# Kernel optimization log

Hardware: AMD Instinct MI355X
Metric: run time of the kernel (lower is better)

## Reference

```python
import jax, jax.numpy as jnp
from jax import lax
import numpy as np

N_ASSETS = 256
BATCH = 512
MAX_WEIGHT = 0.05
N_ITERS = 300       # FISTA iterations (fixed, jit-friendly)
BISECT_ITERS = 60   # bisection iterations for the simplex-box projection
POWER_ITERS = 30    # power iterations for Lipschitz constant


def _project_capped_simplex(v, c):
    """Project rows of v onto {w : sum(w)=1, -c <= w <= c}.

    Finds tau s.t. sum(clip(v - tau, -c, c)) = 1 by bisection (non-diff),
    then recomputes tau exactly from the active-set mask so the projection
    is correctly differentiable (piecewise-linear Jacobian).
    """
    vs = lax.stop_gradient(v)
    lo = jnp.min(vs, axis=-1) - c   # sum = +n*c > 1 here
    hi = jnp.max(vs, axis=-1) + c   # sum = -n*c < 1 here

    def bis(carry, _):
        lo, hi = carry
        mid = 0.5 * (lo + hi)
        s = jnp.sum(jnp.clip(vs - mid[:, None], -c, c), axis=-1)
        lo = jnp.where(s > 1.0, mid, lo)
        hi = jnp.where(s > 1.0, hi, mid)
        return (lo, hi), None

    (lo, hi), _ = lax.scan(bis, (lo, hi), None, length=BISECT_ITERS)
    tau0 = 0.5 * (lo + hi)
    z = vs - tau0[:, None]
    interior = (jnp.abs(z) < c).astype(v.dtype)          # unclipped coords
    k_hi = jnp.sum((z >= c).astype(v.dtype), axis=-1)    # clipped at +c
    k_lo = jnp.sum((z <= -c).astype(v.dtype), axis=-1)   # clipped at -c
    denom = jnp.maximum(jnp.sum(interior, axis=-1), 1.0)
    # exact tau given the (stop-gradient) active set -> correct Jacobian in v
    tau = (jnp.sum(interior * v, axis=-1) + c * (k_hi - k_lo) - 1.0) / denom
    return jnp.clip(v - tau[:, None], -c, c)


def _min_var_weights(covmat_sqrt, c):
    """argmin_w ||A w||^2  s.t. sum(w)=1, -c<=w<=c  (batched FISTA)."""
    B, n, _ = covmat_sqrt.shape
    # Q = A^T A (the objective only depends on A through Q)
    Q = jnp.einsum('bij,bik->bjk', covmat_sqrt, covmat_sqrt)

    # power iteration for lambda_max(Q) -> step size 1/L, L = 2*lambda_max
    u = jnp.ones((B, n), covmat_sqrt.dtype) / jnp.sqrt(jnp.asarray(n, covmat_sqrt.dtype))

    def pit(u, _):
        u = jnp.einsum('bij,bj->bi', Q, u)
        u = u / (jnp.linalg.norm(u, axis=-1, keepdims=True) + 1e-12)
        return u, None

    u, _ = lax.scan(pit, u, None, length=POWER_ITERS)
    lmax = jnp.einsum('bi,bij,bj->b', u, Q, u)
    step = lax.stop_gradient(1.0 / (2.0 * lmax + 1e-12))[:, None]

    w0 = _project_capped_simplex(jnp.full((B, n), 1.0 / n, covmat_sqrt.dtype), c)

    @jax.checkpoint
    def fista(carry, _):
        w, y, t = carry
        g = 2.0 * jnp.einsum('bij,bj->bi', Q, y)
        w_new = _project_capped_simplex(y - step * g, c)
        t_new = 0.5 * (1.0 + jnp.sqrt(1.0 + 4.0 * t * t))
        y_new = w_new + ((t - 1.0) / t_new) * (w_new - w)
        return (w_new, y_new, t_new), None

    t0 = jnp.asarray(1.0, covmat_sqrt.dtype)
    (w, _, _), _ = lax.scan(fista, (w0, w0, t0), None, length=N_ITERS)
    return w


def setup_inputs() -> dict:
    key = jax.random.key(0)
    covmat_sqrt = jax.random.normal(
        key, (BATCH, N_ASSETS, N_ASSETS), dtype=jnp.float32
    ) / np.sqrt(N_ASSETS).astype(np.float32)
    return {"covmat_sqrt": covmat_sqrt}


def reference(covmat_sqrt):
    return _min_var_weights(covmat_sqrt, MAX_WEIGHT)
```

## Files before the change

### kernel.cpp

```cpp
#include <hip/hip_runtime.h>
#include <math.h>


#define NA    256
#define CAPW  0.05f

typedef float v2f __attribute__((ext_vector_type(2)));

template<int CTRL, int RM>
__device__ __forceinline__ float dpp0(float x) {
    return __int_as_float(__builtin_amdgcn_update_dpp(
        0, __float_as_int(x), CTRL, RM, 0xf, true));
}
template<int CTRL, int RM>
__device__ __forceinline__ float dppI(float x, float ident) {
    return __int_as_float(__builtin_amdgcn_update_dpp(
        __float_as_int(ident), __float_as_int(x), CTRL, RM, 0xf, false));
}
__device__ __forceinline__ float bcast63(float x) {
    return __int_as_float(__builtin_amdgcn_readlane(__float_as_int(x), 63));
}
__device__ __forceinline__ float wsum(float x) {
    x += dpp0<0x111, 0xf>(x);
    x += dpp0<0x112, 0xf>(x);
    x += dpp0<0x114, 0xf>(x);
    x += dpp0<0x118, 0xf>(x);
    x += dpp0<0x142, 0xa>(x);
    x += dpp0<0x143, 0xc>(x);
    return bcast63(x);
}
__device__ __forceinline__ float wmin(float x) {
    const float I = 1e30f;
    x = fminf(x, dppI<0x111, 0xf>(x, I));
    x = fminf(x, dppI<0x112, 0xf>(x, I));
    x = fminf(x, dppI<0x114, 0xf>(x, I));
    x = fminf(x, dppI<0x118, 0xf>(x, I));
    x = fminf(x, dppI<0x142, 0xa>(x, I));
    x = fminf(x, dppI<0x143, 0xc>(x, I));
    return bcast63(x);
}
__device__ __forceinline__ float wmax(float x) {
    const float I = -1e30f;
    x = fmaxf(x, dppI<0x111, 0xf>(x, I));
    x = fmaxf(x, dppI<0x112, 0xf>(x, I));
    x = fmaxf(x, dppI<0x114, 0xf>(x, I));
    x = fmaxf(x, dppI<0x118, 0xf>(x, I));
    x = fmaxf(x, dppI<0x142, 0xa>(x, I));
    x = fmaxf(x, dppI<0x143, 0xc>(x, I));
    return bcast63(x);
}

__global__ void __launch_bounds__(512, 2)
markowitz_fista(const float* __restrict__ A, float* __restrict__ out)
{
    __shared__ float A_lds[32 * 256];
    __shared__ float y_lds[256];
    __shared__ float p_lds[8 * 256];
    __shared__ int   done_flag;

    const int tid = threadIdx.x;
    const int b   = blockIdx.x;
    const int r4  = tid & 63;
    const int e   = tid >> 6;
    const int R0  = r4 * 4;
    const int C0  = e * 32;

    const float* __restrict__ Ab = A + (size_t)b * NA * NA;

    v2f q2[4][16];
    #pragma unroll
    for (int a = 0; a < 4; ++a)
        #pragma unroll
        for (int k = 0; k < 16; ++k) q2[a][k] = (v2f){0.0f, 0.0f};

    for (int it = 0; it < 8; ++it) {
        __syncthreads();
        const float4* src = (const float4*)(Ab + it * 32 * 256);
        float4* dst = (float4*)A_lds;
        #pragma unroll
        for (int qd = 0; qd < 4; ++qd) dst[qd * 512 + tid] = src[qd * 512 + tid];
        __syncthreads();
        for (int ii = 0; ii < 32; ++ii) {
            const float* row = A_lds + ii * 256;
            float4 rv = *(const float4*)(row + R0);
            v2f r0 = {rv.x, rv.x}, r1 = {rv.y, rv.y}, r2 = {rv.z, rv.z}, r3 = {rv.w, rv.w};
            #pragma unroll
            for (int cc = 0; cc < 8; ++cc) {
                float4 cv = *(const float4*)(row + C0 + 4 * cc);
                v2f clo = {cv.x, cv.y}, chi = {cv.z, cv.w};
                q2[0][2*cc  ] = __builtin_elementwise_fma(r0, clo, q2[0][2*cc  ]);
                q2[0][2*cc+1] = __builtin_elementwise_fma(r0, chi, q2[0][2*cc+1]);
                q2[1][2*cc  ] = __builtin_elementwise_fma(r1, clo, q2[1][2*cc  ]);
                q2[1][2*cc+1] = __builtin_elementwise_fma(r1, chi, q2[1][2*cc+1]);
                q2[2][2*cc  ] = __builtin_elementwise_fma(r2, clo, q2[2][2*cc  ]);
                q2[2][2*cc+1] = __builtin_elementwise_fma(r2, chi, q2[2][2*cc+1]);
                q2[3][2*cc  ] = __builtin_elementwise_fma(r3, clo, q2[3][2*cc  ]);
                q2[3][2*cc+1] = __builtin_elementwise_fma(r3, chi, q2[3][2*cc+1]);
            }
        }
    }

    auto partials = [&](bool chk) -> bool {
        __syncthreads();
        int fl = chk ? done_flag : 0;
        v2f aL0 = {0,0}, aL1 = {0,0}, aL2 = {0,0}, aL3 = {0,0};
        v2f aH0 = {0,0}, aH1 = {0,0}, aH2 = {0,0}, aH3 = {0,0};
        const float* yv = y_lds + C0;
        #pragma unroll
        for (int cc = 0; cc < 8; ++cc) {
            float4 y4 = *(const float4*)(yv + 4 * cc);
            v2f ylo = {y4.x, y4.y}, yhi = {y4.z, y4.w};
            aL0 = __builtin_elementwise_fma(q2[0][2*cc  ], ylo, aL0);
            aH0 = __builtin_elementwise_fma(q2[0][2*cc+1], yhi, aH0);
            aL1 = __builtin_elementwise_fma(q2[1][2*cc  ], ylo, aL1);
            aH1 = __builtin_elementwise_fma(q2[1][2*cc+1], yhi, aH1);
            aL2 = __builtin_elementwise_fma(q2[2][2*cc  ], ylo, aL2);
            aH2 = __builtin_elementwise_fma(q2[2][2*cc+1], yhi, aH2);
            aL3 = __builtin_elementwise_fma(q2[3][2*cc  ], ylo, aL3);
            aH3 = __builtin_elementwise_fma(q2[3][2*cc+1], yhi, aH3);
        }
        if (fl) return true;
        v2f s0 = aL0 + aH0, s1 = aL1 + aH1, s2 = aL2 + aH2, s3 = aL3 + aH3;
        *(float4*)(p_lds + e * 256 + R0) =
            make_float4(s0.x + s0.y, s1.x + s1.y, s2.x + s2.y, s3.x + s3.y);
        __syncthreads();
        return false;
    };
    auto reduceg = [&]() -> float4 {
        float4 r = *(const float4*)(p_lds + 4 * tid);
        #pragma unroll
        for (int ee = 1; ee < 8; ++ee) {
            float4 pv = *(const float4*)(p_lds + ee * 256 + 4 * tid);
            r.x += pv.x; r.y += pv.y; r.z += pv.z; r.w += pv.w;
        }
        return r;
    };

    if (tid < 64) {
        *(float4*)(y_lds + 4 * tid) = make_float4(0.0625f, 0.0625f, 0.0625f, 0.0625f);
    }
    float u0 = 0.f, u1 = 0.f, u2 = 0.f, u3 = 0.f;
    for (int p = 0; p < 30; ++p) {
        partials(false);
        if (tid < 64) {
            float4 g4 = reduceg();
            float ss = wsum(g4.x*g4.x + g4.y*g4.y + g4.z*g4.z + g4.w*g4.w);
            float inv = 1.0f / (sqrtf(ss) + 1e-12f);
            u0 = g4.x * inv; u1 = g4.y * inv; u2 = g4.z * inv; u3 = g4.w * inv;
            *(float4*)(y_lds + 4 * tid) = make_float4(u0, u1, u2, u3);
        }
    }
    partials(false);

    float step2 = 0.f, t = 1.0f, tau_ws = 0.0f, rm = 0.0f;
    float wa = 0.f, wb = 0.f, wc = 0.f, wd = 0.f;
    float ya = 0.f, yb = 0.f, yc = 0.f, yd = 0.f;
    if (tid < 64) {
        float4 g4 = reduceg();
        float lm = wsum(u0*g4.x + u1*g4.y + u2*g4.z + u3*g4.w);
        float step = 1.0f / (2.0f * lm + 1e-12f);
        step2 = 2.0f * step;
        wa = wb = wc = wd = 1.0f / 256.0f;
        ya = yb = yc = yd = 1.0f / 256.0f;
        *(float4*)(y_lds + 4 * tid) = make_float4(ya, yb, yc, yd);
    }
    if (tid == 0) done_flag = 0;

    for (int itn = 0; itn < 300; ++itn) {
        if (partials(true)) break;
        if (tid < 64) {
            float4 g4 = reduceg();
            float v0 = ya - step2 * g4.x;
            float v1 = yb - step2 * g4.y;
            float v2 = yc - step2 * g4.z;
            float v3 = yd - step2 * g4.w;

            float lo = wmin(fminf(fminf(v0, v1), fminf(v2, v3))) - CAPW;
            float hi = wmax(fmaxf(fmaxf(v0, v1), fmaxf(v2, v3))) + CAPW;
            float tau = fminf(fmaxf(tau_ws, lo), hi);

            float s = 0.f, cnt = 1.f, sm1 = 0.f;
            bool have = false;
            for (int ni = 0; ni < 10; ++ni) {
                float z0 = v0 - tau, z1 = v1 - tau, z2 = v2 - tau, z3 = v3 - tau;
                float c0 = fminf(fmaxf(z0, -CAPW), CAPW);
                float c1 = fminf(fmaxf(z1, -CAPW), CAPW);
                float c2 = fminf(fmaxf(z2, -CAPW), CAPW);
                float c3 = fminf(fmaxf(z3, -CAPW), CAPW);
                s   = wsum(c0 + c1 + c2 + c3);
                cnt = wsum((fabsf(z0) < CAPW ? 1.f : 0.f) +
                           (fabsf(z1) < CAPW ? 1.f : 0.f) +
                           (fabsf(z2) < CAPW ? 1.f : 0.f) +
                           (fabsf(z3) < CAPW ? 1.f : 0.f));
                sm1 = s - 1.0f;
                if (fabsf(sm1) <= 1e-5f) { have = true; break; }
                if (sm1 > 0.0f) lo = tau; else hi = tau;
                float tn2 = tau + sm1 / fmaxf(cnt, 1.0f);
                if (!(tn2 > lo && tn2 < hi)) tn2 = 0.5f * (lo + hi);
                tau = tn2;
            }
            if (!have) {
                float z0 = v0 - tau, z1 = v1 - tau, z2 = v2 - tau, z3 = v3 - tau;
                float c0 = fminf(fmaxf(z0, -CAPW), CAPW);
                float c1 = fminf(fmaxf(z1, -CAPW), CAPW);
                float c2 = fminf(fmaxf(z2, -CAPW), CAPW);
                float c3 = fminf(fmaxf(z3, -CAPW), CAPW);
                s   = wsum(c0 + c1 + c2 + c3);
                cnt = wsum((fabsf(z0) < CAPW ? 1.f : 0.f) +
                           (fabsf(z1) < CAPW ? 1.f : 0.f) +
                           (fabsf(z2) < CAPW ? 1.f : 0.f) +
                           (fabsf(z3) < CAPW ? 1.f : 0.f));
                sm1 = s - 1.0f;
            }
            float tauf = tau + sm1 / fmaxf(cnt, 1.0f);
            tau_ws = tauf;
            float w0n = fminf(fmaxf(v0 - tauf, -CAPW), CAPW);
            float w1n = fminf(fmaxf(v1 - tauf, -CAPW), CAPW);
            float w2n = fminf(fmaxf(v2 - tauf, -CAPW), CAPW);
            float w3n = fminf(fmaxf(v3 - tauf, -CAPW), CAPW);

            float tn = 0.5f * (1.0f + sqrtf(1.0f + 4.0f * t * t));
            float beta = (t - 1.0f) / tn;
            float y0n = w0n + beta * (w0n - wa);
            float y1n = w1n + beta * (w1n - wb);
            float y2n = w2n + beta * (w2n - wc);
            float y3n = w3n + beta * (w3n - wd);

            float dm = fmaxf(fmaxf(fabsf(w0n - wa), fabsf(w1n - wb)),
                             fmaxf(fabsf(w2n - wc), fabsf(w3n - wd)));
            rm = fmaxf(rm, dm);
            if ((itn & 7) == 7) {
                float rmax = wmax(rm);
                if (rmax < 1e-10f && tid == 0) done_flag = 1;
                rm = 0.0f;
            }

            wa = w0n; wb = w1n; wc = w2n; wd = w3n;
            ya = y0n; yb = y1n; yc = y2n; yd = y3n;
            t = tn;
            *(float4*)(y_lds + 4 * tid) = make_float4(ya, yb, yc, yd);
        }
    }

    if (tid < 64) {
        *(float4*)(out + b * 256 + 4 * tid) = make_float4(wa, wb, wc, wd);
    }
}

extern "C" void kernel_launch(void* const* d_in, const int* in_sizes, int n_in,
                              void* d_out, int out_size, void* d_ws, size_t ws_size,
                              hipStream_t stream) {
    (void)in_sizes; (void)n_in; (void)d_ws; (void)ws_size; (void)out_size;
    const float* A = (const float*)d_in[0];
    float* out = (float*)d_out;
    hipLaunchKernelGGL(markowitz_fista, dim3(512), dim3(512), 0, stream, A, out);
}
```

Baseline: 1.056 ms.

## Replicate projection in every wave and double-buffer partials to halve barriers

Every one of the 8 waves now runs the redundant projection and FISTA update itself, so each wave holds the full y vector in registers. The matvec reads y through readlane instead of from LDS. The partial-sum buffer is double-buffered, so each iteration needs one __syncthreads instead of two, and the done-flag broadcast through shared memory is gone. The cost is that all waves execute the serial bisection/Newton projection and the extra readlane instructions, rather than only wave 0 doing it while the others wait.

```diff
diff --git a/kernel.cpp b/kernel.cpp
--- a/kernel.cpp
+++ b/kernel.cpp
@@ -19,6 +19,9 @@
 }
 __device__ __forceinline__ float bcast63(float x) {
     return __int_as_float(__builtin_amdgcn_readlane(__float_as_int(x), 63));
+}
+__device__ __forceinline__ float rlane(float x, int lane) {
+    return __int_as_float(__builtin_amdgcn_readlane(__float_as_int(x), lane));
 }
 __device__ __forceinline__ float wsum(float x) {
     x += dpp0<0x111, 0xf>(x);
@@ -54,9 +57,7 @@
 markowitz_fista(const float* __restrict__ A, float* __restrict__ out)
 {
     __shared__ float A_lds[32 * 256];
-    __shared__ float y_lds[256];
-    __shared__ float p_lds[8 * 256];
-    __shared__ int   done_flag;
+    __shared__ float p_lds[2][8 * 256];
 
     const int tid = threadIdx.x;
     const int b   = blockIdx.x;
@@ -64,6 +65,7 @@
     const int e   = tid >> 6;
     const int R0  = r4 * 4;
     const int C0  = e * 32;
+    const int lb  = __builtin_amdgcn_readfirstlane(e) * 8;
 
     const float* __restrict__ Ab = A + (size_t)b * NA * NA;
 
@@ -100,16 +102,14 @@
         }
     }
 
-    auto partials = [&](bool chk) -> bool {
-        __syncthreads();
-        int fl = chk ? done_flag : 0;
+    auto matvec = [&](float y0, float y1, float y2, float y3, float* buf) {
         v2f aL0 = {0,0}, aL1 = {0,0}, aL2 = {0,0}, aL3 = {0,0};
         v2f aH0 = {0,0}, aH1 = {0,0}, aH2 = {0,0}, aH3 = {0,0};
-        const float* yv = y_lds + C0;
         #pragma unroll
         for (int cc = 0; cc < 8; ++cc) {
-            float4 y4 = *(const float4*)(yv + 4 * cc);
-            v2f ylo = {y4.x, y4.y}, yhi = {y4.z, y4.w};
+            const int L = lb + cc;
+            v2f ylo = { rlane(y0, L), rlane(y1, L) };
+            v2f yhi = { rlane(y2, L), rlane(y3, L) };
             aL0 = __builtin_elementwise_fma(q2[0][2*cc  ], ylo, aL0);
             aH0 = __builtin_elementwise_fma(q2[0][2*cc+1], yhi, aH0);
             aL1 = __builtin_elementwise_fma(q2[1][2*cc  ], ylo, aL1);
@@ -119,131 +119,127 @@
             aL3 = __builtin_elementwise_fma(q2[3][2*cc  ], ylo, aL3);
             aH3 = __builtin_elementwise_fma(q2[3][2*cc+1], yhi, aH3);
         }
-        if (fl) return true;
         v2f s0 = aL0 + aH0, s1 = aL1 + aH1, s2 = aL2 + aH2, s3 = aL3 + aH3;
-        *(float4*)(p_lds + e * 256 + R0) =
+        *(float4*)(buf + e * 256 + R0) =
             make_float4(s0.x + s0.y, s1.x + s1.y, s2.x + s2.y, s3.x + s3.y);
-        __syncthreads();
-        return false;
     };
-    auto reduceg = [&]() -> float4 {
-        float4 r = *(const float4*)(p_lds + 4 * tid);
+    auto reduceg = [&](const float* buf) -> float4 {
+        float4 r = *(const float4*)(buf + R0);
         #pragma unroll
         for (int ee = 1; ee < 8; ++ee) {
-            float4 pv = *(const float4*)(p_lds + ee * 256 + 4 * tid);
+            float4 pv = *(const float4*)(buf + ee * 256 + R0);
             r.x += pv.x; r.y += pv.y; r.z += pv.z; r.w += pv.w;
         }
         return r;
     };
 
+    float u0 = 0.0625f, u1 = 0.0625f, u2 = 0.0625f, u3 = 0.0625f;
+    matvec(u0, u1, u2, u3, p_lds[0]);
+    __syncthreads();
+    int pb = 0;
+    for (int p = 0; p < 30; ++p) {
+        float4 g4 = reduceg(p_lds[pb]);
+        float ss = wsum(g4.x*g4.x + g4.y*g4.y + g4.z*g4.z + g4.w*g4.w);
+        float inv = 1.0f / (sqrtf(ss) + 1e-12f);
+        u0 = g4.x * inv; u1 = g4.y * inv; u2 = g4.z * inv; u3 = g4.w * inv;
+        pb ^= 1;
+        matvec(u0, u1, u2, u3, p_lds[pb]);
+        __syncthreads();
+    }
+    float4 gq = reduceg(p_lds[pb]);
+    float lm = wsum(u0*gq.x + u1*gq.y + u2*gq.z + u3*gq.w);
+    float step  = 1.0f / (2.0f * lm + 1e-12f);
+    float step2 = 2.0f * step;
+
+    float t = 1.0f, tau_ws = 0.0f, rm = 0.0f;
+    float wa = 1.0f/256.0f, wb = 1.0f/256.0f, wc = 1.0f/256.0f, wd = 1.0f/256.0f;
+    float ya = wa, yb = wb, yc = wc, yd = wd;
+
+    pb ^= 1;
+    matvec(ya, yb, yc, yd, p_lds[pb]);
+    __syncthreads();
+
+    for (int itn = 0; itn < 300; ++itn) {
+        float4 g4 = reduceg(p_lds[pb]);
+        float v0 = ya - step2 * g4.x;
+        float v1 = yb - step2 * g4.y;
+        float v2 = yc - step2 * g4.z;
+        float v3 = yd - step2 * g4.w;
+
+        float lo = wmin(fminf(fminf(v0, v1), fminf(v2, v3))) - CAPW;
+        float hi = wmax(fmaxf(fmaxf(v0, v1), fmaxf(v2, v3))) + CAPW;
+        float tau = fminf(fmaxf(tau_ws, lo), hi);
+
+        float s = 0.f, cnt = 1.f, sm1 = 0.f;
+        bool have = false;
+        for (int ni = 0; ni < 10; ++ni) {
+            float z0 = v0 - tau, z1 = v1 - tau, z2 = v2 - tau, z3 = v3 - tau;
+            float c0 = fminf(fmaxf(z0, -CAPW), CAPW);
+            float c1 = fminf(fmaxf(z1, -CAPW), CAPW);
+            float c2 = fminf(fmaxf(z2, -CAPW), CAPW);
+            float c3 = fminf(fmaxf(z3, -CAPW), CAPW);
+            s   = wsum(c0 + c1 + c2 + c3);
+            cnt = wsum((fabsf(z0) < CAPW ? 1.f : 0.f) +
+                       (fabsf(z1) < CAPW ? 1.f : 0.f) +
+                       (fabsf(z2) < CAPW ? 1.f : 0.f) +
+                       (fabsf(z3) < CAPW ? 1.f : 0.f));
+            sm1 = s - 1.0f;
+            if (fabsf(sm1) <= 1e-5f) { have = true; break; }
+            if (sm1 > 0.0f) lo = tau; else hi = tau;
+            float tn2 = tau + sm1 / fmaxf(cnt, 1.0f);
+            if (!(tn2 > lo && tn2 < hi)) tn2 = 0.5f * (lo + hi);
+            tau = tn2;
+        }
+        if (!have) {
+            float z0 = v0 - tau, z1 = v1 - tau, z2 = v2 - tau, z3 = v3 - tau;
+            float c0 = fminf(fmaxf(z0, -CAPW), CAPW);
+            float c1 = fminf(fmaxf(z1, -CAPW), CAPW);
+            float c2 = fminf(fmaxf(z2, -CAPW), CAPW);
+            float c3 = fminf(fmaxf(z3, -CAPW), CAPW);
+            s   = wsum(c0 + c1 + c2 + c3);
+            cnt = wsum((fabsf(z0) < CAPW ? 1.f : 0.f) +
+                       (fabsf(z1) < CAPW ? 1.f : 0.f) +
+                       (fabsf(z2) < CAPW ? 1.f : 0.f) +
+                       (fabsf(z3) < CAPW ? 1.f : 0.f));
+            sm1 = s - 1.0f;
+        }
+        float tauf = tau + sm1 / fmaxf(cnt, 1.0f);
+        tau_ws = tauf;
+        float w0n = fminf(fmaxf(v0 - tauf, -CAPW), CAPW);
+        float w1n = fminf(fmaxf(v1 - tauf, -CAPW), CAPW);
+        float w2n = fminf(fmaxf(v2 - tauf, -CAPW), CAPW);
+        float w3n = fminf(fmaxf(v3 - tauf, -CAPW), CAPW);
+
+        float tn = 0.5f * (1.0f + sqrtf(1.0f + 4.0f * t * t));
+        float beta = (t - 1.0f) / tn;
+        float y0n = w0n + beta * (w0n - wa);
+        float y1n = w1n + beta * (w1n - wb);
+        float y2n = w2n + beta * (w2n - wc);
+        float y3n = w3n + beta * (w3n - wd);
+
+        float dm = fmaxf(fmaxf(fabsf(w0n - wa), fabsf(w1n - wb)),
+                         fmaxf(fabsf(w2n - wc), fabsf(w3n - wd)));
+        rm = fmaxf(rm, dm);
+        bool stop = false;
+        if ((itn & 7) == 7) {
+            float rmax = wmax(rm);
+            stop = (rmax < 1e-10f);
+            rm = 0.0f;
+        }
+
+        wa = w0n; wb = w1n; wc = w2n; wd = w3n;
+        ya = y0n; yb = y1n; yc = y2n; yd = y3n;
+        t = tn;
+
+        if (stop || itn == 299) break;
+
+        pb ^= 1;
+        matvec(ya, yb, yc, yd, p_lds[pb]);
+        __syncthreads();
+    }
+
     if (tid < 64) {
-        *(float4*)(y_lds + 4 * tid) = make_float4(0.0625f, 0.0625f, 0.0625f, 0.0625f);
-    }
-    float u0 = 0.f, u1 = 0.f, u2 = 0.f, u3 = 0.f;
-    for (int p = 0; p < 30; ++p) {
-        partials(false);
-        if (tid < 64) {
-            float4 g4 = reduceg();
-            float ss = wsum(g4.x*g4.x + g4.y*g4.y + g4.z*g4.z + g4.w*g4.w);
-            float inv = 1.0f / (sqrtf(ss) + 1e-12f);
-            u0 = g4.x * inv; u1 = g4.y * inv; u2 = g4.z * inv; u3 = g4.w * inv;
-            *(float4*)(y_lds + 4 * tid) = make_float4(u0, u1, u2, u3);
-        }
-    }
-    partials(false);
-
-    float step2 = 0.f, t = 1.0f, tau_ws = 0.0f, rm = 0.0f;
-    float wa = 0.f, wb = 0.f, wc = 0.f, wd = 0.f;
-    float ya = 0.f, yb = 0.f, yc = 0.f, yd = 0.f;
-    if (tid < 64) {
-        float4 g4 = reduceg();
-        float lm = wsum(u0*g4.x + u1*g4.y + u2*g4.z + u3*g4.w);
-        float step = 1.0f / (2.0f * lm + 1e-12f);
-        step2 = 2.0f * step;
-        wa = wb = wc = wd = 1.0f / 256.0f;
-        ya = yb = yc = yd = 1.0f / 256.0f;
-        *(float4*)(y_lds + 4 * tid) = make_float4(ya, yb, yc, yd);
-    }
-    if (tid == 0) done_flag = 0;
-
-    for (int itn = 0; itn < 300; ++itn) {
-        if (partials(true)) break;
-        if (tid < 64) {
-            float4 g4 = reduceg();
-            float v0 = ya - step2 * g4.x;
-            float v1 = yb - step2 * g4.y;
-            float v2 = yc - step2 * g4.z;
-            float v3 = yd - step2 * g4.w;
-
-            float lo = wmin(fminf(fminf(v0, v1), fminf(v2, v3))) - CAPW;
-            float hi = wmax(fmaxf(fmaxf(v0, v1), fmaxf(v2, v3))) + CAPW;
-            float tau = fminf(fmaxf(tau_ws, lo), hi);
-
-            float s = 0.f, cnt = 1.f, sm1 = 0.f;
-            bool have = false;
-            for (int ni = 0; ni < 10; ++ni) {
-                float z0 = v0 - tau, z1 = v1 - tau, z2 = v2 - tau, z3 = v3 - tau;
-                float c0 = fminf(fmaxf(z0, -CAPW), CAPW);
-                float c1 = fminf(fmaxf(z1, -CAPW), CAPW);
-                float c2 = fminf(fmaxf(z2, -CAPW), CAPW);
-                float c3 = fminf(fmaxf(z3, -CAPW), CAPW);
-                s   = wsum(c0 + c1 + c2 + c3);
-                cnt = wsum((fabsf(z0) < CAPW ? 1.f : 0.f) +
-                           (fabsf(z1) < CAPW ? 1.f : 0.f) +
-                           (fabsf(z2) < CAPW ? 1.f : 0.f) +
-                           (fabsf(z3) < CAPW ? 1.f : 0.f));
-                sm1 = s - 1.0f;
-                if (fabsf(sm1) <= 1e-5f) { have = true; break; }
-                if (sm1 > 0.0f) lo = tau; else hi = tau;
-                float tn2 = tau + sm1 / fmaxf(cnt, 1.0f);
-                if (!(tn2 > lo && tn2 < hi)) tn2 = 0.5f * (lo + hi);
-                tau = tn2;
-            }
-            if (!have) {
-                float z0 = v0 - tau, z1 = v1 - tau, z2 = v2 - tau, z3 = v3 - tau;
-                float c0 = fminf(fmaxf(z0, -CAPW), CAPW);
-                float c1 = fminf(fmaxf(z1, -CAPW), CAPW);
-                float c2 = fminf(fmaxf(z2, -CAPW), CAPW);
-                float c3 = fminf(fmaxf(z3, -CAPW), CAPW);
-                s   = wsum(c0 + c1 + c2 + c3);
-                cnt = wsum((fabsf(z0) < CAPW ? 1.f : 0.f) +
-                           (fabsf(z1) < CAPW ? 1.f : 0.f) +
-                           (fabsf(z2) < CAPW ? 1.f : 0.f) +
-                           (fabsf(z3) < CAPW ? 1.f : 0.f));
-                sm1 = s - 1.0f;
-            }
-            float tauf = tau + sm1 / fmaxf(cnt, 1.0f);
-            tau_ws = tauf;
-            float w0n = fminf(fmaxf(v0 - tauf, -CAPW), CAPW);
-            float w1n = fminf(fmaxf(v1 - tauf, -CAPW), CAPW);
-            float w2n = fminf(fmaxf(v2 - tauf, -CAPW), CAPW);
-            float w3n = fminf(fmaxf(v3 - tauf, -CAPW), CAPW);
-
-            float tn = 0.5f * (1.0f + sqrtf(1.0f + 4.0f * t * t));
-            float beta = (t - 1.0f) / tn;
-            float y0n = w0n + beta * (w0n - wa);
-            float y1n = w1n + beta * (w1n - wb);
-            float y2n = w2n + beta * (w2n - wc);
-            float y3n = w3n + beta * (w3n - wd);
-
-            float dm = fmaxf(fmaxf(fabsf(w0n - wa), fabsf(w1n - wb)),
-                             fmaxf(fabsf(w2n - wc), fabsf(w3n - wd)));
-            rm = fmaxf(rm, dm);
-            if ((itn & 7) == 7) {
-                float rmax = wmax(rm);
-                if (rmax < 1e-10f && tid == 0) done_flag = 1;
-                rm = 0.0f;
-            }
-
-            wa = w0n; wb = w1n; wc = w2n; wd = w3n;
-            ya = y0n; yb = y1n; yc = y2n; yd = y3n;
-            t = tn;
-            *(float4*)(y_lds + 4 * tid) = make_float4(ya, yb, yc, yd);
-        }
-    }
-
-    if (tid < 64) {
-        *(float4*)(out + b * 256 + 4 * tid) = make_float4(wa, wb, wc, wd);
+        *(float4*)(out + b * 256 + R0) = make_float4(wa, wb, wc, wd);
     }
 }
 
```

Result: slower. 1.365 ms (+29.3%).
